# Optimization experiments

Measured on AMD Instinct MI355X. Metric: run time of the kernel, lower is better.

The kernel has to match this reference:

```python
import jax, jax.numpy as jnp
import numpy as np

B, S, D_MODEL = 4, 2048, 1024
N_HEADS, D_HEAD = 16, 64
HIDDEN = N_HEADS * D_HEAD
N_PRIM, RANK = 16, 256
CHUNK = 64  # matches CHUNK_SIZE in the torch module


def setup_inputs() -> dict:
    key = jax.random.key(0)
    ks = jax.random.split(key, 16)
    def n(k, shape, scale=0.02):
        return jax.random.normal(k, shape, dtype=jnp.float32) * scale
    return {
        'x': jax.random.normal(ks[0], (B, S, D_MODEL), dtype=jnp.float32),
        'q_U': n(ks[1], (N_PRIM, D_MODEL, RANK)),
        'q_V': n(ks[2], (N_PRIM, RANK, HIDDEN)),
        'k_U': n(ks[3], (N_PRIM, D_MODEL, RANK)),
        'k_V': n(ks[4], (N_PRIM, RANK, HIDDEN)),
        'v_U': n(ks[5], (N_PRIM, D_MODEL, RANK)),
        'v_V': n(ks[6], (N_PRIM, RANK, HIDDEN)),
        'q_logits': jax.random.normal(ks[7], (N_PRIM,), dtype=jnp.float32),
        'k_logits': jax.random.normal(ks[8], (N_PRIM,), dtype=jnp.float32),
        'v_logits': jax.random.normal(ks[9], (N_PRIM,), dtype=jnp.float32),
        'gate_logits': jax.random.normal(ks[10], (N_PRIM,), dtype=jnp.float32),
        'decay_w': n(ks[11], (N_HEADS, D_MODEL), 0.03),
        'decay_b': jnp.full((N_HEADS,), -2.0, dtype=jnp.float32),
        'out_gate_w': n(ks[12], (HIDDEN, D_MODEL), 0.03),
        'out_proj_w': n(ks[13], (D_MODEL, HIDDEN), 0.03),
        'rms_w': jnp.ones((HIDDEN,), dtype=jnp.float32),
        'top_k': 4,
    }


def _bank_topk_fused(x, U, V, logits, top_k):
    """Top-k fused mixture of low-rank primitives: sum_j w_j * (x @ U_j @ V_j)."""
    w = jax.nn.softmax(logits)                      # [P]
    vals, idx = jax.lax.top_k(w, top_k)             # [k], [k]
    vals = vals / jnp.sum(vals)                     # renormalize selected weights
    Us = U[idx]                                     # [k, d_in, rank]
    Vs = V[idx]                                     # [k, rank, d_out]
    h = jnp.einsum('bsd,kdr->bskr', x, Us)          # low-rank bottleneck
    return jnp.einsum('bskr,kro,k->bso', h, Vs, vals)


def _chunked_scan(q, kv, log_decay):
    """Decay-gated linear recurrence via chunked parallel scan (CHUNK=64).
    q, kv: [B,S,H,D]; log_decay: [B,S,H,1]. Returns [B,S,H,D]."""
    b, s, h, d = q.shape
    nc = s // CHUNK
    # [NC, B, C, H, *] chunked layout for lax.scan over chunks
    qc = jnp.moveaxis(q.reshape(b, nc, CHUNK, h, d), 1, 0)
    kvc = jnp.moveaxis(kv.reshape(b, nc, CHUNK, h, d), 1, 0)
    ldc = jnp.moveaxis(log_decay.reshape(b, nc, CHUNK, h, 1), 1, 0)

    def step(state, inp):
        ld, kvs, qs = inp                            # [B,C,H,1], [B,C,H,D], [B,C,H,D]
        cum = jnp.cumsum(ld, axis=1)                 # cumulative log-decay in chunk
        last = cum[:, -1:]
        kv_shifted = kvs * jnp.exp(last - cum)
        new = jnp.exp(cum - last) * jnp.cumsum(kv_shifted, axis=1)
        chunk_states = state[:, None] * jnp.exp(cum) + new   # [B,C,H,D]
        out = qs * chunk_states
        return chunk_states[:, -1], out

    state0 = jnp.zeros((b, h, d), dtype=jnp.float32)
    _, outs = jax.lax.scan(step, state0, (ldc, kvc, qc))     # [NC,B,C,H,D]
    return jnp.moveaxis(outs, 0, 1).reshape(b, s, h, d)


def reference(x, q_U, q_V, k_U, k_V, v_U, v_V,
              q_logits, k_logits, v_logits, gate_logits,
              decay_w, decay_b, out_gate_w, out_proj_w, rms_w, top_k):
    b, s, _ = x.shape
    h, d = decay_w.shape[0], q_V.shape[-1] // decay_w.shape[0]

    q = _bank_topk_fused(x, q_U, q_V, q_logits, top_k).reshape(b, s, h, d)
    k = _bank_topk_fused(x, k_U, k_V, k_logits, top_k).reshape(b, s, h, d)
    v = _bank_topk_fused(x, v_U, v_V, v_logits, top_k).reshape(b, s, h, d)
    # gate shares the V bank (gate = v_bank.forward_topk_fused with gate weights)
    gate = _bank_topk_fused(x, v_U, v_V, gate_logits, top_k).reshape(b, s, h, d)

    log_decay = -jax.nn.softplus(jnp.einsum('bsd,hd->bsh', x, decay_w) + decay_b)[..., None]  # [B,S,H,1]
    kv = jax.nn.sigmoid(gate) * k * v

    out = _chunked_scan(q, kv.astype(jnp.float32), log_decay.astype(jnp.float32))
    out = out.reshape(b, s, h * d)

    # RMSNorm (torch default eps = finfo.eps for fp32)
    eps = jnp.finfo(jnp.float32).eps
    out = out * jax.lax.rsqrt(jnp.mean(out * out, axis=-1, keepdims=True) + eps) * rms_w
    out = out * jax.nn.sigmoid(jnp.einsum('bsd,od->bso', x, out_gate_w))
    return jnp.einsum('bsh,dh->bsd', out, out_proj_w)
```

## Files before the change

kernel.cpp:

```cpp
#include <hip/hip_runtime.h>
#include <hip/hip_bf16.h>

#define TOK 8192
#define SEQ 2048
#define CT  64
#define NC  32

typedef __attribute__((ext_vector_type(8))) short bf16x8;
typedef __attribute__((ext_vector_type(4))) float f32x4;
typedef unsigned short u16;
typedef unsigned int   u32;

__device__ __forceinline__ u16 f2bf(float f) {
    u32 u = __float_as_uint(f);
    u = (u + 0x7FFFu + ((u >> 16) & 1u)) >> 16;
    return (u16)u;
}
__device__ __forceinline__ float b2f(u16 h) { return __uint_as_float(((u32)h) << 16); }
__device__ __forceinline__ float sigf(float z) { return 1.f / (1.f + __expf(-z)); }

__global__ void topk_kernel(const float* __restrict__ ql, const float* __restrict__ kl,
                            const float* __restrict__ vl, const float* __restrict__ gl,
                            int* __restrict__ sel_idx, float* __restrict__ sel_w)
{
    const int p = threadIdx.x;
    if (p >= 4) return;
    const float* lg = (p == 0) ? ql : (p == 1) ? kl : (p == 2) ? vl : gl;
    float v[16];
    for (int i = 0; i < 16; i++) v[i] = lg[i];
    bool used[16];
    for (int i = 0; i < 16; i++) used[i] = false;
    int idx[4]; float val[4];
    for (int k = 0; k < 4; k++) {
        int bi = -1; float bv = -__builtin_inff();
        for (int i = 0; i < 16; i++)
            if (!used[i] && v[i] > bv) { bv = v[i]; bi = i; }
        used[bi] = true; idx[k] = bi; val[k] = bv;
    }
    const float m = val[0];
    float e[4], s = 0.f;
    for (int k = 0; k < 4; k++) { e[k] = expf(val[k] - m); s += e[k]; }
    for (int k = 0; k < 4; k++) { sel_idx[p*4 + k] = idx[k]; sel_w[p*4 + k] = e[k] / s; }
}

__global__ __launch_bounds__(256)
void f2b_kernel(const float* __restrict__ in, u16* __restrict__ out, int n4)
{
    const int i = blockIdx.x * 256 + threadIdx.x;
    if (i >= n4) return;
    const float4 v = ((const float4*)in)[i];
    __align__(8) u16 t[4] = { f2bf(v.x), f2bf(v.y), f2bf(v.z), f2bf(v.w) };
    ((uint2*)out)[i] = *(const uint2*)t;
}

__global__ __launch_bounds__(256)
void gatherU(const float* __restrict__ qU, const float* __restrict__ kU,
             const float* __restrict__ vU, u16* __restrict__ gU,
             const int* __restrict__ sel_idx_all, const float* __restrict__ sel_w_all)
{
    const int p = blockIdx.z;
    const float* U = (p == 0) ? qU : (p == 1) ? kU : vU;
    const int g = blockIdx.x * 256 + threadIdx.x;
    const int d = g >> 8, kq = g & 255;
    const int k = kq << 2;
    const int s = k >> 8, r = k & 255;
    const int prim = sel_idx_all[p * 4 + s];
    const float wv = sel_w_all[p * 4 + s];
    const float4 v = *(const float4*)(U + (size_t)prim * (1024 * 256) + (size_t)d * 256 + r);
    __align__(8) u16 t[4] = { f2bf(v.x * wv), f2bf(v.y * wv), f2bf(v.z * wv), f2bf(v.w * wv) };
    ((uint2*)(gU + (size_t)p * 1048576))[g] = *(const uint2*)t;
}

__global__ __launch_bounds__(256)
void gatherVT(const float* __restrict__ qV, const float* __restrict__ kV,
              const float* __restrict__ vV, u16* __restrict__ gVT,
              const int* __restrict__ sel_idx_all)
{
    const int p = blockIdx.z;
    const float* V = (p == 0) ? qV : (p == 1) ? kV : vV;
    const int o0 = blockIdx.x * 64;
    const int k0 = blockIdx.y * 64;
    const int s = k0 >> 8, r0 = k0 & 255;
    const int prim = sel_idx_all[p * 4 + s];
    const float* Vb = V + (size_t)prim * (256 * 1024);

    __shared__ float tile[64][68];
    const int tid = threadIdx.x;
    const int rr = tid >> 4, cc = (tid & 15) << 2;
    #pragma unroll
    for (int i = 0; i < 4; i++) {
        const float4 v = *(const float4*)(Vb + (size_t)(r0 + rr + 16 * i) * 1024 + o0 + cc);
        *(float4*)&tile[rr + 16 * i][cc] = v;
    }
    __syncthreads();
    const int oo = tid >> 4, kk = (tid & 15) << 2;
    u16* out = gVT + (size_t)p * 1048576;
    #pragma unroll
    for (int i = 0; i < 4; i++) {
        __align__(8) u16 t[4];
        #pragma unroll
        for (int j = 0; j < 4; j++) t[j] = f2bf(tile[kk + j][oo + 16 * i]);
        *(uint2*)(out + (size_t)(o0 + oo + 16 * i) * 1024 + k0 + kk) = *(const uint2*)t;
    }
}

template<int OUTBF>
__global__ __launch_bounds__(256)
void mfma_gemm(const u16* __restrict__ Asrc, const u16* __restrict__ Bt,
               void* __restrict__ Cout, size_t astride, size_t bstride, size_t cstride)
{
    __shared__ u16 As[128 * 64];
    __shared__ u16 Bs[128 * 64];
    const u16* A = Asrc + (size_t)blockIdx.z * astride;
    const u16* B = Bt + (size_t)blockIdx.z * bstride;
    const int tid  = threadIdx.x;
    const int lane = tid & 63, wave = tid >> 6;
    const int m0 = blockIdx.y * 128, n0 = blockIdx.x * 128;
    const int wm = (wave >> 1) * 64, wn = (wave & 1) * 64;

    f32x4 acc[4][4];
    #pragma unroll
    for (int i = 0; i < 4; i++)
        #pragma unroll
        for (int j = 0; j < 4; j++) acc[i][j] = (f32x4)0.f;

    for (int k0 = 0; k0 < 1024; k0 += 64) {
        __syncthreads();
        #pragma unroll
        for (int it = 0; it < 4; it++) {
            const int c   = it * 256 + tid;
            const int row = c >> 3, j = c & 7;
            const int g   = j ^ (row & 7);
            const u16* ga = A + (size_t)(m0 + row) * 1024 + k0 + g * 8;
            __builtin_amdgcn_global_load_lds(
                (const __attribute__((address_space(1))) u32*)ga,
                (__attribute__((address_space(3))) u32*)&As[(it * 256 + wave * 64) * 8],
                16, 0, 0);
            const u16* gb = B + (size_t)(n0 + row) * 1024 + k0 + g * 8;
            __builtin_amdgcn_global_load_lds(
                (const __attribute__((address_space(1))) u32*)gb,
                (__attribute__((address_space(3))) u32*)&Bs[(it * 256 + wave * 64) * 8],
                16, 0, 0);
        }
        __syncthreads();
        #pragma unroll
        for (int ks = 0; ks < 2; ks++) {
            bf16x8 af[4], bfr[4];
            const int gk = ks * 4 + (lane >> 4);
            #pragma unroll
            for (int mi = 0; mi < 4; mi++) {
                const int r  = wm + mi * 16 + (lane & 15);
                const int ja = gk ^ (r & 7);
                af[mi] = *(const bf16x8*)&As[r * 64 + ja * 8];
                const int rn = wn + mi * 16 + (lane & 15);
                const int jb = gk ^ (rn & 7);
                bfr[mi] = *(const bf16x8*)&Bs[rn * 64 + jb * 8];
            }
            #pragma unroll
            for (int mi = 0; mi < 4; mi++)
                #pragma unroll
                for (int ni = 0; ni < 4; ni++)
                    acc[mi][ni] = __builtin_amdgcn_mfma_f32_16x16x32_bf16(
                        af[mi], bfr[ni], acc[mi][ni], 0, 0, 0);
        }
    }
    const int col_l = lane & 15, row_l = (lane >> 4) * 4;
    if (OUTBF) {
        u16* C = (u16*)Cout + (size_t)blockIdx.z * cstride;
        #pragma unroll
        for (int mi = 0; mi < 4; mi++)
            #pragma unroll
            for (int ni = 0; ni < 4; ni++)
                #pragma unroll
                for (int i = 0; i < 4; i++) {
                    const int r  = m0 + wm + mi * 16 + row_l + i;
                    const int cn = n0 + wn + ni * 16 + col_l;
                    C[(size_t)r * 1024 + cn] = f2bf(acc[mi][ni][i]);
                }
    } else {
        float* C = (float*)Cout + (size_t)blockIdx.z * cstride;
        #pragma unroll
        for (int mi = 0; mi < 4; mi++)
            #pragma unroll
            for (int ni = 0; ni < 4; ni++)
                #pragma unroll
                for (int i = 0; i < 4; i++) {
                    const int r  = m0 + wm + mi * 16 + row_l + i;
                    const int cn = n0 + wn + ni * 16 + col_l;
                    C[(size_t)r * 1024 + cn] = acc[mi][ni][i];
                }
    }
}

__global__ __launch_bounds__(256)
void decay_kernel(const float* __restrict__ x, const float* __restrict__ dw,
                  const float* __restrict__ db, float* __restrict__ dec)
{
    const int wave = threadIdx.x >> 6, lane = threadIdx.x & 63;
    const int t = blockIdx.x * 4 + wave;
    const float4* x4 = (const float4*)(x + (size_t)t * 1024);
    float4 xv[4];
    #pragma unroll
    for (int i = 0; i < 4; i++) xv[i] = x4[lane + 64 * i];
    float p[16];
    #pragma unroll
    for (int h = 0; h < 16; h++) {
        const float4* w4 = (const float4*)(dw + (size_t)h * 1024);
        float s = 0.f;
        #pragma unroll
        for (int i = 0; i < 4; i++) {
            const float4 wv = w4[lane + 64 * i];
            s = fmaf(xv[i].x, wv.x, fmaf(xv[i].y, wv.y,
                fmaf(xv[i].z, wv.z, fmaf(xv[i].w, wv.w, s))));
        }
        p[h] = s;
    }
    #pragma unroll
    for (int off = 32; off > 0; off >>= 1)
        #pragma unroll
        for (int h = 0; h < 16; h++) p[h] += __shfl_xor(p[h], off);
    if (lane == 0) {
        #pragma unroll
        for (int h = 0; h < 16; h++)
            dec[(size_t)t * 16 + h] = 1.f / (1.f + __expf(p[h] + db[h]));
    }
}

__global__ __launch_bounds__(64)
void scan1(const u16* __restrict__ Kq, const u16* __restrict__ Vq, const u16* __restrict__ Gq,
           const float* __restrict__ dec, float* __restrict__ Lc, float* __restrict__ Pc)
{
    const int c = blockIdx.x & 31, h = (blockIdx.x >> 5) & 15, b = blockIdx.x >> 9;
    const int d = threadIdx.x;
    const size_t t0 = (size_t)b * SEQ + c * CT;
    const size_t base = t0 * 1024 + h * 64 + d;
    const u16* kp = Kq + base;
    const u16* vp = Vq + base;
    const u16* gp = Gq + base;
    const float* dp = dec + t0 * 16 + h;
    float s = 0.f, P = 1.f;
    #pragma unroll 4
    for (int t = 0; t < CT; t++) {
        const size_t o = (size_t)t * 1024;
        const float a  = dp[t * 16];
        const float kv = b2f(kp[o]) * b2f(vp[o]) * sigf(b2f(gp[o]));
        s = fmaf(a, s, kv);
        P *= a;
    }
    const int ci = (b * 16 + h) * NC + c;
    Lc[(size_t)ci * 64 + d] = s;
    if (d == 0) Pc[ci] = P;
}

__global__ __launch_bounds__(64)
void scan2(const float* __restrict__ Lc, const float* __restrict__ Pc, float* __restrict__ Ic)
{
    const int bh = blockIdx.x, d = threadIdx.x;
    float S = 0.f;
    for (int c = 0; c < NC; c++) {
        const int ci = bh * NC + c;
        Ic[(size_t)ci * 64 + d] = S;
        S = fmaf(Pc[ci], S, Lc[(size_t)ci * 64 + d]);
    }
}

__global__ __launch_bounds__(64)
void scan3(const u16* __restrict__ Qq, const u16* __restrict__ Kq,
           const u16* __restrict__ Vq, const u16* __restrict__ Gq,
           const float* __restrict__ dec, const float* __restrict__ Ic,
           float* __restrict__ out)
{
    const int c = blockIdx.x & 31, h = (blockIdx.x >> 5) & 15, b = blockIdx.x >> 9;
    const int d = threadIdx.x;
    const size_t t0 = (size_t)b * SEQ + c * CT;
    const size_t base = t0 * 1024 + h * 64 + d;
    const u16* qp = Qq + base;
    const u16* kp = Kq + base;
    const u16* vp = Vq + base;
    const u16* gp = Gq + base;
    const float* dp = dec + t0 * 16 + h;
    const int ci = (b * 16 + h) * NC + c;
    float s = Ic[(size_t)ci * 64 + d];
    #pragma unroll 4
    for (int t = 0; t < CT; t++) {
        const size_t o = (size_t)t * 1024;
        const float a  = dp[t * 16];
        const float kv = b2f(kp[o]) * b2f(vp[o]) * sigf(b2f(gp[o]));
        s = fmaf(a, s, kv);
        out[base + o] = b2f(qp[o]) * s;
    }
}

__global__ __launch_bounds__(256)
void rms_gate(const float* __restrict__ att, const u16* __restrict__ gpre,
              const float* __restrict__ rmsw, u16* __restrict__ o)
{
    const size_t t = blockIdx.x;
    const int tid = threadIdx.x;
    const float4 a = ((const float4*)(att + t * 1024))[tid];
    float ss = a.x*a.x + a.y*a.y + a.z*a.z + a.w*a.w;
    #pragma unroll
    for (int d = 32; d > 0; d >>= 1) ss += __shfl_down(ss, d);
    __shared__ float red[4];
    if ((tid & 63) == 0) red[tid >> 6] = ss;
    __syncthreads();
    const float tot = red[0] + red[1] + red[2] + red[3];
    const float scale = rsqrtf(tot * (1.0f / 1024.0f) + 1.1920929e-7f);
    const ushort4 g4 = ((const ushort4*)(gpre + t * 1024))[tid];
    const float4 w   = ((const float4*)rmsw)[tid];
    __align__(8) u16 r[4];
    r[0] = f2bf(a.x * scale * w.x * sigf(b2f(g4.x)));
    r[1] = f2bf(a.y * scale * w.y * sigf(b2f(g4.y)));
    r[2] = f2bf(a.z * scale * w.z * sigf(b2f(g4.z)));
    r[3] = f2bf(a.w * scale * w.w * sigf(b2f(g4.w)));
    ((uint2*)(o + t * 1024))[tid] = *(const uint2*)r;
}

extern "C" void kernel_launch(void* const* d_in, const int* in_sizes, int n_in,
                              void* d_out, int out_size, void* d_ws, size_t ws_size,
                              hipStream_t stream)
{
    const float* x    = (const float*)d_in[0];
    const float* qU   = (const float*)d_in[1];
    const float* qV   = (const float*)d_in[2];
    const float* kU   = (const float*)d_in[3];
    const float* kV   = (const float*)d_in[4];
    const float* vU   = (const float*)d_in[5];
    const float* vV   = (const float*)d_in[6];
    const float* ql   = (const float*)d_in[7];
    const float* kl   = (const float*)d_in[8];
    const float* vl   = (const float*)d_in[9];
    const float* gl   = (const float*)d_in[10];
    const float* dw   = (const float*)d_in[11];
    const float* db   = (const float*)d_in[12];
    const float* ogw  = (const float*)d_in[13];
    const float* opw  = (const float*)d_in[14];
    const float* rmsw = (const float*)d_in[15];

    char* w = (char*)d_ws;
    int*   sel_idx = (int*)  (w + 0);
    float* sel_w   = (float*)(w + 64);
    float* dec     = (float*)(w + 128);
    u16*   WT      = (u16*)  (w + 524544);
    u16*   xb      = (u16*)  (w + 8913152);
    u16*   ogwb    = (u16*)  (w + 25690368);
    u16*   opwb    = (u16*)  (w + 27787520);
    u16*   QKVG    = (u16*)  (w + 29884672);
    u16*   GPRE    = (u16*)  (w + 96993536);
    u16*   RMSO    = (u16*)  (w + 113770752);
    float* ATT     = (float*)(w + 130547968);
    float* Lc      = (float*)(w + 164102400);
    float* Ic      = (float*)(w + 164626688);
    float* Pc      = (float*)(w + 165150976);
    u16*   gU      = QKVG;
    u16*   gVT     = QKVG + 4 * 1048576;

    topk_kernel<<<1, 64, 0, stream>>>(ql, kl, vl, gl, sel_idx, sel_w);

    f2b_kernel<<<8192, 256, 0, stream>>>(x,   xb,   2097152);
    f2b_kernel<<<1024, 256, 0, stream>>>(ogw, ogwb, 262144);
    f2b_kernel<<<1024, 256, 0, stream>>>(opw, opwb, 262144);

    gatherU <<<dim3(1024, 1, 4), 256, 0, stream>>>(qU, kU, vU, gU, sel_idx, sel_w);
    gatherVT<<<dim3(16, 16, 4),  256, 0, stream>>>(qV, kV, vV, gVT, sel_idx);

    mfma_gemm<1><<<dim3(8, 8, 4), 256, 0, stream>>>(gVT, gU, WT,
                                                    (size_t)1048576, (size_t)1048576,
                                                    (size_t)1048576);

    mfma_gemm<1><<<dim3(8, 64, 4), 256, 0, stream>>>(xb, WT, QKVG,
                                                     (size_t)0, (size_t)1048576,
                                                     (size_t)8388608);

    decay_kernel<<<2048, 256, 0, stream>>>(x, dw, db, dec);

    scan1<<<2048, 64, 0, stream>>>(QKVG + 8388608, QKVG + 16777216, QKVG + 25165824,
                                   dec, Lc, Pc);
    scan2<<<64, 64, 0, stream>>>(Lc, Pc, Ic);
    scan3<<<2048, 64, 0, stream>>>(QKVG, QKVG + 8388608, QKVG + 16777216, QKVG + 25165824,
                                   dec, Ic, ATT);

    mfma_gemm<1><<<dim3(8, 64, 1), 256, 0, stream>>>(xb, ogwb, GPRE, 0, 0, 0);

    rms_gate<<<8192, 256, 0, stream>>>(ATT, GPRE, rmsw, RMSO);

    mfma_gemm<0><<<dim3(8, 64, 1), 256, 0, stream>>>(RMSO, opwb, (float*)d_out, 0, 0, 0);
}
```

Before: 414.4 us.

## Fuse setup kernels, batch gate GEMM with QKVG, remap tiles per XCD, bf16 scan output

Merges the top-k selection into the gather kernel and the three fp32-to-bf16 casts into one launch. A dedicated 64x64-tile GEMM builds the combined bank weights. The out-gate projection becomes a fifth batch entry of the QKVG GEMM by placing its weights right after WT. Workgroups of the big GEMM are remapped so each XCD gets a contiguous band of M rows for L2 reuse. The scan writes its output as bf16 instead of fp32 to halve that traffic, at the cost of some precision before the RMSNorm.

```diff
diff --git a/kernel.cpp b/kernel.cpp
--- a/kernel.cpp
+++ b/kernel.cpp
@@ -19,89 +19,159 @@
 __device__ __forceinline__ float b2f(u16 h) { return __uint_as_float(((u32)h) << 16); }
 __device__ __forceinline__ float sigf(float z) { return 1.f / (1.f + __expf(-z)); }
 
-__global__ void topk_kernel(const float* __restrict__ ql, const float* __restrict__ kl,
-                            const float* __restrict__ vl, const float* __restrict__ gl,
-                            int* __restrict__ sel_idx, float* __restrict__ sel_w)
-{
-    const int p = threadIdx.x;
-    if (p >= 4) return;
-    const float* lg = (p == 0) ? ql : (p == 1) ? kl : (p == 2) ? vl : gl;
+__device__ __forceinline__ void topk4(const float* __restrict__ lg, int* idx, float* wv)
+{
     float v[16];
+    #pragma unroll
     for (int i = 0; i < 16; i++) v[i] = lg[i];
     bool used[16];
+    #pragma unroll
     for (int i = 0; i < 16; i++) used[i] = false;
-    int idx[4]; float val[4];
+    float val[4];
+    #pragma unroll
     for (int k = 0; k < 4; k++) {
-        int bi = -1; float bv = -__builtin_inff();
+        int bi = 0; float bv = -3.0e38f;
+        #pragma unroll
         for (int i = 0; i < 16; i++)
             if (!used[i] && v[i] > bv) { bv = v[i]; bi = i; }
         used[bi] = true; idx[k] = bi; val[k] = bv;
     }
-    const float m = val[0];
     float e[4], s = 0.f;
-    for (int k = 0; k < 4; k++) { e[k] = expf(val[k] - m); s += e[k]; }
-    for (int k = 0; k < 4; k++) { sel_idx[p*4 + k] = idx[k]; sel_w[p*4 + k] = e[k] / s; }
-}
-
-__global__ __launch_bounds__(256)
-void f2b_kernel(const float* __restrict__ in, u16* __restrict__ out, int n4)
+    #pragma unroll
+    for (int k = 0; k < 4; k++) { e[k] = expf(val[k] - val[0]); s += e[k]; }
+    #pragma unroll
+    for (int k = 0; k < 4; k++) wv[k] = e[k] / s;
+}
+
+__global__ __launch_bounds__(256)
+void f2b_all(const float* __restrict__ x, const float* __restrict__ ogw,
+             const float* __restrict__ opw,
+             u16* __restrict__ xb, u16* __restrict__ ogwb, u16* __restrict__ opwb)
 {
     const int i = blockIdx.x * 256 + threadIdx.x;
-    if (i >= n4) return;
-    const float4 v = ((const float4*)in)[i];
+    const float* src; u16* dst; int off;
+    if (i < 2097152)      { src = x;   dst = xb;   off = i; }
+    else if (i < 2359296) { src = ogw; dst = ogwb; off = i - 2097152; }
+    else                  { src = opw; dst = opwb; off = i - 2359296; }
+    const float4 v = ((const float4*)src)[off];
     __align__(8) u16 t[4] = { f2bf(v.x), f2bf(v.y), f2bf(v.z), f2bf(v.w) };
-    ((uint2*)out)[i] = *(const uint2*)t;
-}
-
-__global__ __launch_bounds__(256)
-void gatherU(const float* __restrict__ qU, const float* __restrict__ kU,
-             const float* __restrict__ vU, u16* __restrict__ gU,
-             const int* __restrict__ sel_idx_all, const float* __restrict__ sel_w_all)
-{
-    const int p = blockIdx.z;
-    const float* U = (p == 0) ? qU : (p == 1) ? kU : vU;
-    const int g = blockIdx.x * 256 + threadIdx.x;
-    const int d = g >> 8, kq = g & 255;
-    const int k = kq << 2;
-    const int s = k >> 8, r = k & 255;
-    const int prim = sel_idx_all[p * 4 + s];
-    const float wv = sel_w_all[p * 4 + s];
-    const float4 v = *(const float4*)(U + (size_t)prim * (1024 * 256) + (size_t)d * 256 + r);
-    __align__(8) u16 t[4] = { f2bf(v.x * wv), f2bf(v.y * wv), f2bf(v.z * wv), f2bf(v.w * wv) };
-    ((uint2*)(gU + (size_t)p * 1048576))[g] = *(const uint2*)t;
-}
-
-__global__ __launch_bounds__(256)
-void gatherVT(const float* __restrict__ qV, const float* __restrict__ kV,
-              const float* __restrict__ vV, u16* __restrict__ gVT,
-              const int* __restrict__ sel_idx_all)
-{
-    const int p = blockIdx.z;
-    const float* V = (p == 0) ? qV : (p == 1) ? kV : vV;
-    const int o0 = blockIdx.x * 64;
-    const int k0 = blockIdx.y * 64;
-    const int s = k0 >> 8, r0 = k0 & 255;
-    const int prim = sel_idx_all[p * 4 + s];
-    const float* Vb = V + (size_t)prim * (256 * 1024);
-
-    __shared__ float tile[64][68];
+    ((uint2*)dst)[off] = *(const uint2*)t;
+}
+
+__global__ __launch_bounds__(256)
+void gather_all(const float* __restrict__ qU, const float* __restrict__ kU,
+                const float* __restrict__ vU,
+                const float* __restrict__ qV, const float* __restrict__ kV,
+                const float* __restrict__ vV,
+                const float* __restrict__ ql, const float* __restrict__ kl,
+                const float* __restrict__ vl, const float* __restrict__ gl,
+                u16* __restrict__ gU, u16* __restrict__ gVT)
+{
+    const int z = blockIdx.z;
+    const int p = z & 3;
+    const float* lg = (p == 0) ? ql : (p == 1) ? kl : (p == 2) ? vl : gl;
+    int idx[4]; float wsel[4];
+    topk4(lg, idx, wsel);
     const int tid = threadIdx.x;
-    const int rr = tid >> 4, cc = (tid & 15) << 2;
-    #pragma unroll
-    for (int i = 0; i < 4; i++) {
-        const float4 v = *(const float4*)(Vb + (size_t)(r0 + rr + 16 * i) * 1024 + o0 + cc);
-        *(float4*)&tile[rr + 16 * i][cc] = v;
-    }
-    __syncthreads();
-    const int oo = tid >> 4, kk = (tid & 15) << 2;
-    u16* out = gVT + (size_t)p * 1048576;
-    #pragma unroll
-    for (int i = 0; i < 4; i++) {
-        __align__(8) u16 t[4];
-        #pragma unroll
-        for (int j = 0; j < 4; j++) t[j] = f2bf(tile[kk + j][oo + 16 * i]);
-        *(uint2*)(out + (size_t)(o0 + oo + 16 * i) * 1024 + k0 + kk) = *(const uint2*)t;
-    }
+
+    if (z < 4) {
+        const float* V = (p == 0) ? qV : (p == 1) ? kV : vV;
+        const int o0 = blockIdx.x * 64, k0 = blockIdx.y * 64;
+        const int s = k0 >> 8, r0 = k0 & 255;
+        const float* Vb = V + (size_t)idx[s] * (256 * 1024);
+        __shared__ float tile[64][68];
+        const int rr = tid >> 4, cc = (tid & 15) << 2;
+        #pragma unroll
+        for (int i = 0; i < 4; i++) {
+            const float4 v = *(const float4*)(Vb + (size_t)(r0 + rr + 16 * i) * 1024 + o0 + cc);
+            *(float4*)&tile[rr + 16 * i][cc] = v;
+        }
+        __syncthreads();
+        const int oo = tid >> 4, kk = (tid & 15) << 2;
+        u16* out = gVT + (size_t)p * 1048576;
+        #pragma unroll
+        for (int i = 0; i < 4; i++) {
+            __align__(8) u16 t[4];
+            #pragma unroll
+            for (int j = 0; j < 4; j++) t[j] = f2bf(tile[kk + j][oo + 16 * i]);
+            *(uint2*)(out + (size_t)(o0 + oo + 16 * i) * 1024 + k0 + kk) = *(const uint2*)t;
+        }
+    } else {
+        const float* U = (p == 0) ? qU : (p == 1) ? kU : vU;
+        const int d0 = blockIdx.x * 64, k0 = blockIdx.y * 64;
+        const int s = k0 >> 8, r0 = k0 & 255;
+        const float* Ub = U + (size_t)idx[s] * (1024 * 256);
+        const float wq = wsel[s];
+        u16* out = gU + (size_t)p * 1048576;
+        const int rr = tid >> 4, cc = (tid & 15) << 2;
+        #pragma unroll
+        for (int i = 0; i < 4; i++) {
+            const float4 v = *(const float4*)(Ub + (size_t)(d0 + rr + 16 * i) * 256 + r0 + cc);
+            __align__(8) u16 t[4] = { f2bf(v.x * wq), f2bf(v.y * wq),
+                                      f2bf(v.z * wq), f2bf(v.w * wq) };
+            *(uint2*)(out + (size_t)(d0 + rr + 16 * i) * 1024 + k0 + cc) = *(const uint2*)t;
+        }
+    }
+}
+
+__global__ __launch_bounds__(256)
+void mfma_gemm64(const u16* __restrict__ Asrc, const u16* __restrict__ Bsrc,
+                 u16* __restrict__ Cout)
+{
+    __shared__ u16 As[64 * 64];
+    __shared__ u16 Bs[64 * 64];
+    const int z = blockIdx.z;
+    const u16* A = Asrc + (size_t)z * 1048576;
+    const u16* B = Bsrc + (size_t)z * 1048576;
+    u16* C = Cout + (size_t)z * 1048576;
+    const int tid = threadIdx.x, lane = tid & 63, wave = tid >> 6;
+    const int m0 = blockIdx.y * 64, n0 = blockIdx.x * 64;
+    const int wn = wave * 16;
+
+    f32x4 acc[4];
+    #pragma unroll
+    for (int i = 0; i < 4; i++) acc[i] = (f32x4)0.f;
+
+    for (int k0 = 0; k0 < 1024; k0 += 64) {
+        __syncthreads();
+        #pragma unroll
+        for (int it = 0; it < 2; it++) {
+            const int c   = it * 256 + tid;
+            const int row = c >> 3, j = c & 7;
+            const int g   = j ^ (row & 7);
+            const u16* ga = A + (size_t)(m0 + row) * 1024 + k0 + g * 8;
+            __builtin_amdgcn_global_load_lds(
+                (const __attribute__((address_space(1))) u32*)ga,
+                (__attribute__((address_space(3))) u32*)&As[(it * 256 + wave * 64) * 8],
+                16, 0, 0);
+            const u16* gb = B + (size_t)(n0 + row) * 1024 + k0 + g * 8;
+            __builtin_amdgcn_global_load_lds(
+                (const __attribute__((address_space(1))) u32*)gb,
+                (__attribute__((address_space(3))) u32*)&Bs[(it * 256 + wave * 64) * 8],
+                16, 0, 0);
+        }
+        __syncthreads();
+        #pragma unroll
+        for (int ks = 0; ks < 2; ks++) {
+            const int gk = ks * 4 + (lane >> 4);
+            const int rn = wn + (lane & 15);
+            const int jb = gk ^ (rn & 7);
+            const bf16x8 bfr = *(const bf16x8*)&Bs[rn * 64 + jb * 8];
+            #pragma unroll
+            for (int mi = 0; mi < 4; mi++) {
+                const int rm = mi * 16 + (lane & 15);
+                const int ja = gk ^ (rm & 7);
+                const bf16x8 af = *(const bf16x8*)&As[rm * 64 + ja * 8];
+                acc[mi] = __builtin_amdgcn_mfma_f32_16x16x32_bf16(af, bfr, acc[mi], 0, 0, 0);
+            }
+        }
+    }
+    const int col_l = lane & 15, row_l = (lane >> 4) * 4;
+    #pragma unroll
+    for (int mi = 0; mi < 4; mi++)
+        #pragma unroll
+        for (int i = 0; i < 4; i++)
+            C[(size_t)(m0 + mi * 16 + row_l + i) * 1024 + n0 + wn + col_l] = f2bf(acc[mi][i]);
 }
 
 template<int OUTBF>
@@ -111,11 +181,16 @@
 {
     __shared__ u16 As[128 * 64];
     __shared__ u16 Bs[128 * 64];
-    const u16* A = Asrc + (size_t)blockIdx.z * astride;
-    const u16* B = Bt + (size_t)blockIdx.z * bstride;
+    const int flat = blockIdx.x + 8 * (blockIdx.y + 64 * blockIdx.z);
+    const int xcd = flat & 7;
+    const int r   = flat >> 3;
+    const int nb = r & 7, mlocal = (r >> 3) & 7, zb = r >> 6;
+    const int m0 = (xcd * 8 + mlocal) * 128, n0 = nb * 128;
+
+    const u16* A = Asrc + (size_t)zb * astride;
+    const u16* B = Bt   + (size_t)zb * bstride;
     const int tid  = threadIdx.x;
     const int lane = tid & 63, wave = tid >> 6;
-    const int m0 = blockIdx.y * 128, n0 = blockIdx.x * 128;
     const int wm = (wave >> 1) * 64, wn = (wave & 1) * 64;
 
     f32x4 acc[4][4];
@@ -149,9 +224,9 @@
             const int gk = ks * 4 + (lane >> 4);
             #pragma unroll
             for (int mi = 0; mi < 4; mi++) {
-                const int r  = wm + mi * 16 + (lane & 15);
-                const int ja = gk ^ (r & 7);
-                af[mi] = *(const bf16x8*)&As[r * 64 + ja * 8];
+                const int rr  = wm + mi * 16 + (lane & 15);
+                const int ja = gk ^ (rr & 7);
+                af[mi] = *(const bf16x8*)&As[rr * 64 + ja * 8];
                 const int rn = wn + mi * 16 + (lane & 15);
                 const int jb = gk ^ (rn & 7);
                 bfr[mi] = *(const bf16x8*)&Bs[rn * 64 + jb * 8];
@@ -166,28 +241,28 @@
     }
     const int col_l = lane & 15, row_l = (lane >> 4) * 4;
     if (OUTBF) {
-        u16* C = (u16*)Cout + (size_t)blockIdx.z * cstride;
+        u16* C = (u16*)Cout + (size_t)zb * cstride;
         #pragma unroll
         for (int mi = 0; mi < 4; mi++)
             #pragma unroll
             for (int ni = 0; ni < 4; ni++)
                 #pragma unroll
                 for (int i = 0; i < 4; i++) {
-                    const int r  = m0 + wm + mi * 16 + row_l + i;
+                    const int rw  = m0 + wm + mi * 16 + row_l + i;
                     const int cn = n0 + wn + ni * 16 + col_l;
-                    C[(size_t)r * 1024 + cn] = f2bf(acc[mi][ni][i]);
+                    C[(size_t)rw * 1024 + cn] = f2bf(acc[mi][ni][i]);
                 }
     } else {
-        float* C = (float*)Cout + (size_t)blockIdx.z * cstride;
+        float* C = (float*)Cout + (size_t)zb * cstride;
         #pragma unroll
         for (int mi = 0; mi < 4; mi++)
             #pragma unroll
             for (int ni = 0; ni < 4; ni++)
                 #pragma unroll
                 for (int i = 0; i < 4; i++) {
-                    const int r  = m0 + wm + mi * 16 + row_l + i;
+                    const int rw  = m0 + wm + mi * 16 + row_l + i;
                     const int cn = n0 + wn + ni * 16 + col_l;
-                    C[(size_t)r * 1024 + cn] = acc[mi][ni][i];
+                    C[(size_t)rw * 1024 + cn] = acc[mi][ni][i];
                 }
     }
 }
@@ -268,7 +343,7 @@
 void scan3(const u16* __restrict__ Qq, const u16* __restrict__ Kq,
            const u16* __restrict__ Vq, const u16* __restrict__ Gq,
            const float* __restrict__ dec, const float* __restrict__ Ic,
-           float* __restrict__ out)
+           u16* __restrict__ attb)
 {
     const int c = blockIdx.x & 31, h = (blockIdx.x >> 5) & 15, b = blockIdx.x >> 9;
     const int d = threadIdx.x;
@@ -287,18 +362,19 @@
         const float a  = dp[t * 16];
         const float kv = b2f(kp[o]) * b2f(vp[o]) * sigf(b2f(gp[o]));
         s = fmaf(a, s, kv);
-        out[base + o] = b2f(qp[o]) * s;
-    }
-}
-
-__global__ __launch_bounds__(256)
-void rms_gate(const float* __restrict__ att, const u16* __restrict__ gpre,
+        attb[base + o] = f2bf(b2f(qp[o]) * s);
+    }
+}
+
+__global__ __launch_bounds__(256)
+void rms_gate(const u16* __restrict__ attb, const u16* __restrict__ gpre,
               const float* __restrict__ rmsw, u16* __restrict__ o)
 {
     const size_t t = blockIdx.x;
     const int tid = threadIdx.x;
-    const float4 a = ((const float4*)(att + t * 1024))[tid];
-    float ss = a.x*a.x + a.y*a.y + a.z*a.z + a.w*a.w;
+    const ushort4 a4 = ((const ushort4*)(attb + t * 1024))[tid];
+    const float ax = b2f(a4.x), ay = b2f(a4.y), az = b2f(a4.z), aw = b2f(a4.w);
+    float ss = ax*ax + ay*ay + az*az + aw*aw;
     #pragma unroll
     for (int d = 32; d > 0; d >>= 1) ss += __shfl_down(ss, d);
     __shared__ float red[4];
@@ -309,10 +385,10 @@
     const ushort4 g4 = ((const ushort4*)(gpre + t * 1024))[tid];
     const float4 w   = ((const float4*)rmsw)[tid];
     __align__(8) u16 r[4];
-    r[0] = f2bf(a.x * scale * w.x * sigf(b2f(g4.x)));
-    r[1] = f2bf(a.y * scale * w.y * sigf(b2f(g4.y)));
-    r[2] = f2bf(a.z * scale * w.z * sigf(b2f(g4.z)));
-    r[3] = f2bf(a.w * scale * w.w * sigf(b2f(g4.w)));
+    r[0] = f2bf(ax * scale * w.x * sigf(b2f(g4.x)));
+    r[1] = f2bf(ay * scale * w.y * sigf(b2f(g4.y)));
+    r[2] = f2bf(az * scale * w.z * sigf(b2f(g4.z)));
+    r[3] = f2bf(aw * scale * w.w * sigf(b2f(g4.w)));
     ((uint2*)(o + t * 1024))[tid] = *(const uint2*)r;
 }
 
@@ -338,37 +414,29 @@
     const float* rmsw = (const float*)d_in[15];
 
     char* w = (char*)d_ws;
-    int*   sel_idx = (int*)  (w + 0);
-    float* sel_w   = (float*)(w + 64);
-    float* dec     = (float*)(w + 128);
-    u16*   WT      = (u16*)  (w + 524544);
-    u16*   xb      = (u16*)  (w + 8913152);
-    u16*   ogwb    = (u16*)  (w + 25690368);
-    u16*   opwb    = (u16*)  (w + 27787520);
-    u16*   QKVG    = (u16*)  (w + 29884672);
-    u16*   GPRE    = (u16*)  (w + 96993536);
-    u16*   RMSO    = (u16*)  (w + 113770752);
-    float* ATT     = (float*)(w + 130547968);
-    float* Lc      = (float*)(w + 164102400);
-    float* Ic      = (float*)(w + 164626688);
-    float* Pc      = (float*)(w + 165150976);
-    u16*   gU      = QKVG;
-    u16*   gVT     = QKVG + 4 * 1048576;
-
-    topk_kernel<<<1, 64, 0, stream>>>(ql, kl, vl, gl, sel_idx, sel_w);
-
-    f2b_kernel<<<8192, 256, 0, stream>>>(x,   xb,   2097152);
-    f2b_kernel<<<1024, 256, 0, stream>>>(ogw, ogwb, 262144);
-    f2b_kernel<<<1024, 256, 0, stream>>>(opw, opwb, 262144);
-
-    gatherU <<<dim3(1024, 1, 4), 256, 0, stream>>>(qU, kU, vU, gU, sel_idx, sel_w);
-    gatherVT<<<dim3(16, 16, 4),  256, 0, stream>>>(qV, kV, vV, gVT, sel_idx);
-
-    mfma_gemm<1><<<dim3(8, 8, 4), 256, 0, stream>>>(gVT, gU, WT,
-                                                    (size_t)1048576, (size_t)1048576,
-                                                    (size_t)1048576);
-
-    mfma_gemm<1><<<dim3(8, 64, 4), 256, 0, stream>>>(xb, WT, QKVG,
+    float* dec  = (float*)(w + 0);
+    u16*   WT   = (u16*)  (w + 524288);
+    u16*   xb   = (u16*)  (w + 11010048);
+    u16*   opwb = (u16*)  (w + 27787264);
+    u16*   QKVG = (u16*)  (w + 29884416);
+    u16*   RMSO = (u16*)  (w + 113770496);
+    u16*   ATTb = (u16*)  (w + 130547712);
+    float* Lc   = (float*)(w + 147324928);
+    float* Ic   = (float*)(w + 147849216);
+    float* Pc   = (float*)(w + 148373504);
+    u16*   gU   = QKVG;
+    u16*   gVT  = QKVG + 4194304;
+    u16*   ogwb = WT + 4 * 1048576;
+    u16*   GPRE = QKVG + 4 * 8388608;
+
+    f2b_all<<<10240, 256, 0, stream>>>(x, ogw, opw, xb, ogwb, opwb);
+
+    gather_all<<<dim3(16, 16, 8), 256, 0, stream>>>(qU, kU, vU, qV, kV, vV,
+                                                    ql, kl, vl, gl, gU, gVT);
+
+    mfma_gemm64<<<dim3(16, 16, 4), 256, 0, stream>>>(gVT, gU, WT);
+
+    mfma_gemm<1><<<dim3(8, 64, 5), 256, 0, stream>>>(xb, WT, QKVG,
                                                      (size_t)0, (size_t)1048576,
                                                      (size_t)8388608);
 
@@ -378,11 +446,9 @@
                                    dec, Lc, Pc);
     scan2<<<64, 64, 0, stream>>>(Lc, Pc, Ic);
     scan3<<<2048, 64, 0, stream>>>(QKVG, QKVG + 8388608, QKVG + 16777216, QKVG + 25165824,
-                                   dec, Ic, ATT);
-
-    mfma_gemm<1><<<dim3(8, 64, 1), 256, 0, stream>>>(xb, ogwb, GPRE, 0, 0, 0);
-
-    rms_gate<<<8192, 256, 0, stream>>>(ATT, GPRE, rmsw, RMSO);
+                                   dec, Ic, ATTb);
+
+    rms_gate<<<8192, 256, 0, stream>>>(ATTb, GPRE, rmsw, RMSO);
 
     mfma_gemm<0><<<dim3(8, 64, 1), 256, 0, stream>>>(RMSO, opwb, (float*)d_out, 0, 0, 0);
 }
```

Result: no change. 411.7 us (-0.7%).
